# Kernel optimization log

Measured on AMD Instinct MI355X. Metric: run time of the kernel, lower is better.

## Reference

```python
import jax, jax.numpy as jnp
import numpy as np

N_NUM = 8
N_CAT = 4
CARD = 100
D_NUM = 16
D_CAT = 16
D_OUT = N_NUM * D_NUM + N_CAT * D_CAT  # 192
D_HID = 256
TEMP = 1.0


def setup_inputs() -> dict:
    key = jax.random.key(0)
    ks = jax.random.split(key, 12)
    B, N = 512, 131072
    x_num = jax.random.normal(ks[0], (B, N_NUM), dtype=jnp.float32)
    x_cat = jax.random.randint(ks[1], (B, N_CAT), 0, CARD)
    cand_x_num = jax.random.normal(ks[2], (N, N_NUM), dtype=jnp.float32)
    cand_x_cat = jax.random.randint(ks[3], (N, N_CAT), 0, CARD)
    cand_y = jax.random.uniform(ks[4], (N, 10), dtype=jnp.float32)
    s = 0.05
    W_num = jax.random.normal(ks[5], (N_NUM, D_NUM), dtype=jnp.float32) * s
    b_num = jax.random.normal(ks[6], (N_NUM, D_NUM), dtype=jnp.float32) * s
    emb = jax.random.normal(ks[7], (N_CAT, CARD, D_CAT), dtype=jnp.float32) * s
    W1 = jax.random.normal(ks[8], (D_OUT, D_HID), dtype=jnp.float32) * s
    b1 = jnp.zeros((D_HID,), dtype=jnp.float32)
    W2 = jax.random.normal(ks[9], (D_HID, D_OUT), dtype=jnp.float32) * s
    b2 = jnp.zeros((D_OUT,), dtype=jnp.float32)
    return dict(x_num=x_num, x_cat=x_cat, cand_x_num=cand_x_num,
                cand_x_cat=cand_x_cat, cand_y=cand_y, W_num=W_num, b_num=b_num,
                emb=emb, W1=W1, b1=b1, W2=W2, b2=b2)


def _encode(x_num, x_cat, W_num, b_num, emb):
    # per-numerical-feature linear embedding: [B, n_num, d_num]
    num_e = x_num[:, :, None] * W_num[None] + b_num[None]
    # categorical lookup: emb[f, x_cat[:, f]] -> [B, n_cat, d_cat]
    cat_e = emb[jnp.arange(N_CAT)[None, :], x_cat]
    B = x_num.shape[0]
    return jnp.concatenate([num_e.reshape(B, -1), cat_e.reshape(B, -1)], axis=-1)


def _block(z, W1, b1, W2, b2):
    # residual MLP block: d_out -> hidden -> d_out
    return z + jax.nn.relu(z @ W1 + b1) @ W2 + b2


def reference(x_num, x_cat, cand_x_num, cand_x_cat, cand_y,
              W_num, b_num, emb, W1, b1, W2, b2):
    x = _encode(x_num, x_cat, W_num, b_num, emb)            # [B, d]
    c = _encode(cand_x_num, cand_x_cat, W_num, b_num, emb)  # [N, d]
    x = _block(x, W1, b1, W2, b2)
    c = _block(c, W1, b1, W2, b2)
    d2 = (jnp.sum(x * x, axis=-1)[:, None] + jnp.sum(c * c, axis=-1)[None, :]
          - 2.0 * (x @ c.T))
    dist = jnp.sqrt(jnp.maximum(d2, 0.0)) / TEMP            # [B, N]
    probs = jax.nn.softmax(-dist, axis=-1)
    return probs @ cand_y                                    # [B, 10]
```

## Files before the change

### kernel.cpp

```cpp
#include <hip/hip_runtime.h>
#include <hip/hip_bf16.h>

typedef __bf16 bf16;
typedef __attribute__((ext_vector_type(8))) __bf16 bf16x8;
typedef __attribute__((ext_vector_type(4))) __bf16 bf16x4;
typedef __attribute__((ext_vector_type(4))) float f32x4;

#define NQ     512
#define NC     131072
#define DIM    192
#define HID    256
#define NY     10
#define NSLICE 512

#define KL2E   2.0813689810056077f
#define N2KL2E -4.1627379620112154f

#define OFF_W1B 0u
#define OFF_W2B (OFF_W1B + 49152u)
#define OFF_XE8 (OFF_W2B + 49152u)
#define OFF_X2  (OFF_XE8 + 98304u)
#define OFF_CE8 (OFF_X2 + 2048u)
#define OFF_C2  (OFF_CE8 + 25165824u)
#define OFF_ACC (OFF_C2 + 524288u)
#define OFF_YB  (OFF_ACC + 262144u)

static __device__ __forceinline__ unsigned pk4(float a, float b, float c, float d) {
  unsigned w = __builtin_amdgcn_cvt_pk_fp8_f32(a, b, 0, false);
  w = __builtin_amdgcn_cvt_pk_fp8_f32(c, d, w, true);
  return w;
}

__global__ __launch_bounds__(256) void k_prep(const float* __restrict__ W1,
                                              const float* __restrict__ W2,
                                              const float* __restrict__ cy,
                                              unsigned char* __restrict__ W1B8,
                                              unsigned char* __restrict__ W2B8,
                                              bf16* __restrict__ YB,
                                              float* __restrict__ ACC) {
  if (blockIdx.x < 384) {
    int idx = blockIdx.x * 256 + threadIdx.x;
    if (idx < 192 * 256) {
      int k = idx / 256, n = idx % 256;
      int p = (k >> 5) * 4 + ((k >> 3) & 3);
      int pk = __builtin_amdgcn_cvt_pk_fp8_f32(W1[idx], W1[idx], 0, false);
      W1B8[((size_t)(p * 256 + n)) * 8 + (k & 7)] = (unsigned char)(pk & 0xff);
    } else {
      int i2 = idx - 192 * 256;
      int k = i2 / 192, n = i2 % 192;
      int p = (k >> 5) * 4 + ((k >> 3) & 3);
      int pk = __builtin_amdgcn_cvt_pk_fp8_f32(W2[i2], W2[i2], 0, false);
      W2B8[((size_t)(p * 192 + n)) * 8 + (k & 7)] = (unsigned char)(pk & 0xff);
    }
  } else if (blockIdx.x < 1408) {
    int u = (blockIdx.x - 384) * 256 + threadIdx.x;
    int p32 = u >> 6, lane6 = u & 63;
    int qq = lane6 >> 4, l15 = lane6 & 15;
    bf16x8 v;
#pragma unroll
    for (int jj = 0; jj < 8; jj++) {
      int cand = p32 * 32 + qq * 8 + jj;
      float x = (l15 < 10) ? cy[(size_t)cand * NY + l15] : (l15 == 10 ? 1.f : 0.f);
      v[jj] = (bf16)x;
    }
    *(bf16x8*)&YB[(size_t)u * 8] = v;
  } else {
    int idx = (blockIdx.x - 1408) * 256 + threadIdx.x;
    f32x4 z = {0.f, 0.f, 0.f, 0.f};
    *(f32x4*)&ACC[idx * 4] = z;
  }
}

__global__ __launch_bounds__(256, 4) void k_encode(
    const float* __restrict__ xnq, const int* __restrict__ xcq,
    const float* __restrict__ xnc, const int* __restrict__ xcc,
    const float* __restrict__ Wn, const float* __restrict__ bn,
    const float* __restrict__ emb, const float* __restrict__ b1,
    const float* __restrict__ b2, const unsigned char* __restrict__ W1B8,
    const unsigned char* __restrict__ W2B8, unsigned char* __restrict__ ce8,
    unsigned char* __restrict__ xe8, float* __restrict__ x2v,
    float* __restrict__ c2v) {
  __shared__ alignas(16) unsigned char zt8[64][208];
  __shared__ alignas(16) unsigned char hth8[64][264];
  __shared__ float n2l[64];

  const int t = threadIdx.x;
  const bool isq = blockIdx.x < 8;
  const int row0 = (isq ? blockIdx.x : blockIdx.x - 8) * 64;
  const float* __restrict__ xn = isq ? xnq : xnc;
  const int* __restrict__ xc = isq ? xcq : xcc;
  const int lane = t & 63, w = t >> 6;
  const int l15 = lane & 15, q = lane >> 4;

  if (t < 64) n2l[t] = 0.f;

  {
    const int g = row0 + lane;
    float2 xv2 = *(const float2*)&xn[(size_t)g * 8 + 2 * w];
    int cv = xc[g * 4 + w];
#pragma unroll
    for (int f01 = 0; f01 < 2; f01++) {
      int f = 2 * w + f01;
      float xv = f01 ? xv2.y : xv2.x;
      float zz[16];
#pragma unroll
      for (int i = 0; i < 4; i++) {
        f32x4 wv = *(const f32x4*)&Wn[f * 16 + i * 4];
        f32x4 bv = *(const f32x4*)&bn[f * 16 + i * 4];
#pragma unroll
        for (int u = 0; u < 4; u++) zz[i * 4 + u] = xv * wv[u] + bv[u];
      }
      uint4 pk;
      pk.x = pk4(zz[0], zz[1], zz[2], zz[3]);
      pk.y = pk4(zz[4], zz[5], zz[6], zz[7]);
      pk.z = pk4(zz[8], zz[9], zz[10], zz[11]);
      pk.w = pk4(zz[12], zz[13], zz[14], zz[15]);
      *(uint4*)&zt8[lane][f * 16] = pk;
    }
    const float* er = &emb[(size_t)(w * 100 + cv) * 16];
    f32x4 e0 = *(const f32x4*)&er[0];
    f32x4 e1 = *(const f32x4*)&er[4];
    f32x4 e2 = *(const f32x4*)&er[8];
    f32x4 e3 = *(const f32x4*)&er[12];
    uint4 pk;
    pk.x = pk4(e0[0], e0[1], e0[2], e0[3]);
    pk.y = pk4(e1[0], e1[1], e1[2], e1[3]);
    pk.z = pk4(e2[0], e2[1], e2[2], e2[3]);
    pk.w = pk4(e3[0], e3[1], e3[2], e3[3]);
    *(uint4*)&zt8[lane][128 + w * 16] = pk;
  }
  __syncthreads();

  f32x4 z4 = {0.f, 0.f, 0.f, 0.f};

  {
    f32x4 acc1[4][4];
#pragma unroll
    for (int mi = 0; mi < 4; mi++)
#pragma unroll
      for (int ni = 0; ni < 4; ni++) acc1[mi][ni] = z4;
#pragma unroll 2
    for (int kk = 0; kk < 192; kk += 32) {
      long a[4], b[4];
#pragma unroll
      for (int mi = 0; mi < 4; mi++)
        a[mi] = *(const long*)&zt8[mi * 16 + l15][kk + q * 8];
      const unsigned char* wp = &W1B8[(size_t)(((kk >> 5) * 4 + q) * 256 + w * 64 + l15) * 8];
#pragma unroll
      for (int ni = 0; ni < 4; ni++)
        b[ni] = *(const long*)&wp[ni * 128];
#pragma unroll
      for (int mi = 0; mi < 4; mi++)
#pragma unroll
        for (int ni = 0; ni < 4; ni++)
          acc1[mi][ni] = __builtin_amdgcn_mfma_f32_16x16x32_fp8_fp8(b[ni], a[mi], acc1[mi][ni], 0, 0, 0);
    }
#pragma unroll
    for (int ni = 0; ni < 4; ni++) {
      f32x4 bb = *(const f32x4*)&b1[w * 64 + ni * 16 + q * 4];
#pragma unroll
      for (int mi = 0; mi < 4; mi++) {
        float h0 = acc1[mi][ni][0] + bb[0]; h0 = h0 > 0.f ? h0 : 0.f;
        float h1 = acc1[mi][ni][1] + bb[1]; h1 = h1 > 0.f ? h1 : 0.f;
        float h2 = acc1[mi][ni][2] + bb[2]; h2 = h2 > 0.f ? h2 : 0.f;
        float h3 = acc1[mi][ni][3] + bb[3]; h3 = h3 > 0.f ? h3 : 0.f;
        *(unsigned*)&hth8[mi * 16 + l15][w * 64 + ni * 16 + q * 4] = pk4(h0, h1, h2, h3);
      }
    }
  }
  __syncthreads();

  f32x4 acc2[4][3];
#pragma unroll
  for (int mi = 0; mi < 4; mi++)
#pragma unroll
    for (int ni = 0; ni < 3; ni++) acc2[mi][ni] = z4;
#pragma unroll 2
  for (int kk = 0; kk < 256; kk += 32) {
    long a[4], b[3];
#pragma unroll
    for (int mi = 0; mi < 4; mi++)
      a[mi] = *(const long*)&hth8[mi * 16 + l15][kk + q * 8];
    const unsigned char* wp = &W2B8[(size_t)(((kk >> 5) * 4 + q) * 192 + w * 48 + l15) * 8];
#pragma unroll
    for (int ni = 0; ni < 3; ni++)
      b[ni] = *(const long*)&wp[ni * 128];
#pragma unroll
    for (int mi = 0; mi < 4; mi++)
#pragma unroll
      for (int ni = 0; ni < 3; ni++)
        acc2[mi][ni] = __builtin_amdgcn_mfma_f32_16x16x32_fp8_fp8(b[ni], a[mi], acc2[mi][ni], 0, 0, 0);
  }

  {
    float nrm[4];
#pragma unroll
    for (int mi = 0; mi < 4; mi++) nrm[mi] = 0.f;
#pragma unroll
    for (int ni = 0; ni < 3; ni++) {
      const int n0 = w * 48 + ni * 16 + q * 4;
      f32x4 bb = *(const f32x4*)&b2[n0];
#pragma unroll
      for (int mi = 0; mi < 4; mi++) {
        const int rr = mi * 16 + l15;
        unsigned old = *(const unsigned*)&zt8[rr][n0];
        float v0 = __builtin_amdgcn_cvt_f32_fp8((int)old, 0) + acc2[mi][ni][0] + bb[0];
        float v1 = __builtin_amdgcn_cvt_f32_fp8((int)old, 1) + acc2[mi][ni][1] + bb[1];
        float v2 = __builtin_amdgcn_cvt_f32_fp8((int)old, 2) + acc2[mi][ni][2] + bb[2];
        float v3 = __builtin_amdgcn_cvt_f32_fp8((int)old, 3) + acc2[mi][ni][3] + bb[3];
        unsigned pkw = pk4(v0, v1, v2, v3);
        *(unsigned*)&zt8[rr][n0] = pkw;
        float r0 = __builtin_amdgcn_cvt_f32_fp8((int)pkw, 0);
        float r1 = __builtin_amdgcn_cvt_f32_fp8((int)pkw, 1);
        float r2 = __builtin_amdgcn_cvt_f32_fp8((int)pkw, 2);
        float r3 = __builtin_amdgcn_cvt_f32_fp8((int)pkw, 3);
        nrm[mi] += r0 * r0 + r1 * r1 + r2 * r2 + r3 * r3;
      }
    }
#pragma unroll
    for (int mi = 0; mi < 4; mi++) {
      float s = nrm[mi];
      s += __shfl_xor(s, 16);
      s += __shfl_xor(s, 32);
      if (lane < 16) atomicAdd(&n2l[mi * 16 + l15], s);
    }
  }
  __syncthreads();

  if (isq) {
    for (int cc = w; cc < 24; cc += 4) {
      long v = *(const long*)&zt8[lane][cc * 8];
      *(long*)&xe8[((size_t)cc * NQ + row0 + lane) * 8] = v;
    }
    if (t < 64) x2v[row0 + t] = n2l[t] * KL2E;
  } else {
    unsigned int* dst = (unsigned int*)(ce8 + (size_t)row0 * DIM);
#pragma unroll
    for (int i = 0; i < 12; i++) {
      int j = t + 256 * i;
      int r = j / 48, cb = (j - r * 48) * 4;
      dst[j] = *(const unsigned int*)&zt8[r][cb];
    }
    if (t < 64) c2v[row0 + t] = n2l[t] * KL2E;
  }
}

__global__ __launch_bounds__(256, 4) void k_dist(
    const unsigned char* __restrict__ xe8, const float* __restrict__ x2v,
    const unsigned char* __restrict__ ce8, const float* __restrict__ c2v,
    const bf16* __restrict__ YB, float* __restrict__ ACC) {
  __shared__ alignas(16) unsigned char ct8[2][64][208];
  __shared__ alignas(16) bf16 ET[4][16][72];

  const int t = threadIdx.x;
  const int slice = blockIdx.x & (NSLICE - 1);
  const int half = blockIdx.x >> 9;
  const int n0 = slice * 256;
  const int qh = half * 256;
  const int lane = t & 63, w = t >> 6;
  const int l15 = lane & 15, q = lane >> 4;
  const int qbase = qh + w * 64;
  const int sr = t >> 2, squ = t & 3;

  f32x4 z4 = {0.f, 0.f, 0.f, 0.f};
  f32x4 oacc[4];
#pragma unroll
  for (int nq = 0; nq < 4; nq++) oacc[nq] = z4;

  float x2a[4];
#pragma unroll
  for (int nq = 0; nq < 4; nq++) x2a[nq] = x2v[qbase + nq * 16 + l15];

  {
    const uint4* src = (const uint4*)(ce8 + (size_t)(n0 + sr) * DIM + squ * 48);
    uint4* dst = (uint4*)&ct8[0][sr][squ * 48];
#pragma unroll
    for (int i = 0; i < 3; i++) dst[i] = src[i];
  }

#pragma unroll 1
  for (int c = 0; c < 4; ++c) {
    const int cb = c & 1;
    uint4 pf0, pf1, pf2;
    if (c < 3) {
      const uint4* src = (const uint4*)(ce8 + (size_t)(n0 + (c + 1) * 64 + sr) * DIM + squ * 48);
      pf0 = src[0]; pf1 = src[1]; pf2 = src[2];
    }
    __syncthreads();

    f32x4 acc[4][4];
#pragma unroll
    for (int mc = 0; mc < 4; mc++)
#pragma unroll
      for (int nq = 0; nq < 4; nq++) acc[mc][nq] = z4;

#pragma unroll 1
    for (int kk = 0; kk < 192; kk += 32) {
      long a[4], b[4];
#pragma unroll
      for (int mc = 0; mc < 4; mc++)
        a[mc] = *(const long*)&ct8[cb][mc * 16 + l15][kk + q * 8];
      const unsigned char* xp = &xe8[(size_t)(((kk >> 5) * 4 + q) * NQ + qbase + l15) * 8];
#pragma unroll
      for (int nq = 0; nq < 4; nq++)
        b[nq] = *(const long*)&xp[nq * 128];
#pragma unroll
      for (int mc = 0; mc < 4; mc++)
#pragma unroll
        for (int nq = 0; nq < 4; nq++)
          acc[mc][nq] = __builtin_amdgcn_mfma_f32_16x16x32_fp8_fp8(a[mc], b[nq], acc[mc][nq], 0, 0, 0);
    }

    bf16x8 yf[2];
#pragma unroll
    for (int kb = 0; kb < 2; kb++)
      yf[kb] = *(const bf16x8*)&YB[((size_t)((slice * 8) + c * 2 + kb) * 64 + lane) * 8];
    f32x4 c2r[4];
#pragma unroll
    for (int mc = 0; mc < 4; mc++)
      c2r[mc] = *(const f32x4*)&c2v[n0 + c * 64 + mc * 16 + q * 4];

#pragma unroll
    for (int nq = 0; nq < 4; ++nq) {
#pragma unroll
      for (int mc = 0; mc < 4; mc++) {
        bf16x4 ev;
#pragma unroll
        for (int r = 0; r < 4; r++) {
          float d2 = __builtin_fmaf(N2KL2E, acc[mc][nq][r], x2a[nq] + c2r[mc][r]);
          ev[r] = (bf16)__builtin_amdgcn_exp2f(-__builtin_amdgcn_sqrtf(__builtin_fabsf(d2)));
        }
        *(bf16x4*)&ET[w][l15][mc * 16 + q * 4] = ev;
      }
#pragma unroll
      for (int kb = 0; kb < 2; kb++) {
        bf16x8 a = *(const bf16x8*)&ET[w][l15][kb * 32 + q * 8];
        oacc[nq] = __builtin_amdgcn_mfma_f32_16x16x32_bf16(a, yf[kb], oacc[nq], 0, 0, 0);
      }
    }

    if (c < 3) {
      uint4* dst = (uint4*)&ct8[cb ^ 1][sr][squ * 48];
      dst[0] = pf0; dst[1] = pf1; dst[2] = pf2;
    }
  }

  {
    const int i8 = blockIdx.x & 7;
    float* pb = ACC + ((size_t)i8 * NQ + qbase) * 16 + q * 64 + l15;
    if (l15 < 11) {
#pragma unroll
      for (int nq = 0; nq < 4; nq++)
#pragma unroll
        for (int r = 0; r < 4; r++)
          atomicAdd(pb + nq * 256 + r * 16, oacc[nq][r]);
    }
  }
}

__global__ __launch_bounds__(256) void k_norm(const float* __restrict__ ACC,
                                              float* __restrict__ out) {
  int u = blockIdx.x * 256 + threadIdx.x;
  int qy = u >> 4, y = u & 15;
  if (y < 10) {
    float o = 0.f, l = 0.f;
#pragma unroll
    for (int i = 0; i < 8; i++) {
      o += ACC[((size_t)i * NQ + qy) * 16 + y];
      l += ACC[((size_t)i * NQ + qy) * 16 + 10];
    }
    out[qy * NY + y] = o / l;
  }
}

extern "C" void kernel_launch(void* const* d_in, const int* in_sizes, int n_in,
                              void* d_out, int out_size, void* d_ws, size_t ws_size,
                              hipStream_t stream) {
  (void)in_sizes; (void)n_in; (void)out_size; (void)ws_size;
  const float* x_num = (const float*)d_in[0];
  const int*   x_cat = (const int*)d_in[1];
  const float* c_num = (const float*)d_in[2];
  const int*   c_cat = (const int*)d_in[3];
  const float* c_y   = (const float*)d_in[4];
  const float* W_num = (const float*)d_in[5];
  const float* b_num = (const float*)d_in[6];
  const float* emb   = (const float*)d_in[7];
  const float* W1    = (const float*)d_in[8];
  const float* b1    = (const float*)d_in[9];
  const float* W2    = (const float*)d_in[10];
  const float* b2    = (const float*)d_in[11];
  float* out = (float*)d_out;

  char* ws = (char*)d_ws;
  unsigned char* W1B8 = (unsigned char*)(ws + OFF_W1B);
  unsigned char* W2B8 = (unsigned char*)(ws + OFF_W2B);
  unsigned char* xe8  = (unsigned char*)(ws + OFF_XE8);
  float* x2v = (float*)(ws + OFF_X2);
  unsigned char* ce8  = (unsigned char*)(ws + OFF_CE8);
  float* c2v = (float*)(ws + OFF_C2);
  float* ACC = (float*)(ws + OFF_ACC);
  bf16*  YB  = (bf16*)(ws + OFF_YB);

  k_prep<<<dim3(1472), dim3(256), 0, stream>>>(W1, W2, c_y, W1B8, W2B8, YB, ACC);
  k_encode<<<dim3(8 + NC / 64), dim3(256), 0, stream>>>(
      x_num, x_cat, c_num, c_cat, W_num, b_num, emb, b1, b2, W1B8, W2B8,
      ce8, xe8, x2v, c2v);
  k_dist<<<dim3(2 * NSLICE), dim3(256), 0, stream>>>(xe8, x2v, ce8, c2v, YB, ACC);
  k_norm<<<dim3(32), dim3(256), 0, stream>>>(ACC, out);
}
```

Before: 167.0 us.

## Split distance MFMA into halves, remap slices, stage atomics through LDS

The distance GEMM is split into two query halves, so only an 4x2 accumulator tile is live at once. This cuts VGPR pressure, which matters under the 4-waves launch bound. Block-to-slice mapping is permuted so consecutive blocks touch different candidate regions. The final partial sums are transposed through shared memory so each thread issues 11 contiguous atomics instead of scattered ones. The added syncs and LDS traffic are small, but the x operand is now reloaded per half.

```diff
diff --git a/kernel.cpp b/kernel.cpp
--- a/kernel.cpp
+++ b/kernel.cpp
@@ -253,8 +253,10 @@
   __shared__ alignas(16) bf16 ET[4][16][72];
 
   const int t = threadIdx.x;
-  const int slice = blockIdx.x & (NSLICE - 1);
-  const int half = blockIdx.x >> 9;
+  const int raw = blockIdx.x;
+  const int half = raw >> 9;
+  const int r9 = raw & (NSLICE - 1);
+  const int slice = (r9 & 7) * 64 + (r9 >> 3);
   const int n0 = slice * 256;
   const int qh = half * 256;
   const int lane = t & 63, w = t >> 6;
@@ -288,29 +290,6 @@
     }
     __syncthreads();
 
-    f32x4 acc[4][4];
-#pragma unroll
-    for (int mc = 0; mc < 4; mc++)
-#pragma unroll
-      for (int nq = 0; nq < 4; nq++) acc[mc][nq] = z4;
-
-#pragma unroll 1
-    for (int kk = 0; kk < 192; kk += 32) {
-      long a[4], b[4];
-#pragma unroll
-      for (int mc = 0; mc < 4; mc++)
-        a[mc] = *(const long*)&ct8[cb][mc * 16 + l15][kk + q * 8];
-      const unsigned char* xp = &xe8[(size_t)(((kk >> 5) * 4 + q) * NQ + qbase + l15) * 8];
-#pragma unroll
-      for (int nq = 0; nq < 4; nq++)
-        b[nq] = *(const long*)&xp[nq * 128];
-#pragma unroll
-      for (int mc = 0; mc < 4; mc++)
-#pragma unroll
-        for (int nq = 0; nq < 4; nq++)
-          acc[mc][nq] = __builtin_amdgcn_mfma_f32_16x16x32_fp8_fp8(a[mc], b[nq], acc[mc][nq], 0, 0, 0);
-    }
-
     bf16x8 yf[2];
 #pragma unroll
     for (int kb = 0; kb < 2; kb++)
@@ -321,21 +300,48 @@
       c2r[mc] = *(const f32x4*)&c2v[n0 + c * 64 + mc * 16 + q * 4];
 
 #pragma unroll
-    for (int nq = 0; nq < 4; ++nq) {
-#pragma unroll
-      for (int mc = 0; mc < 4; mc++) {
-        bf16x4 ev;
-#pragma unroll
-        for (int r = 0; r < 4; r++) {
-          float d2 = __builtin_fmaf(N2KL2E, acc[mc][nq][r], x2a[nq] + c2r[mc][r]);
-          ev[r] = (bf16)__builtin_amdgcn_exp2f(-__builtin_amdgcn_sqrtf(__builtin_fabsf(d2)));
+    for (int nqh = 0; nqh < 2; nqh++) {
+      f32x4 acc[4][2];
+#pragma unroll
+      for (int mc = 0; mc < 4; mc++)
+#pragma unroll
+        for (int j = 0; j < 2; j++) acc[mc][j] = z4;
+
+#pragma unroll 2
+      for (int kk = 0; kk < 192; kk += 32) {
+        long a[4], b[2];
+#pragma unroll
+        for (int mc = 0; mc < 4; mc++)
+          a[mc] = *(const long*)&ct8[cb][mc * 16 + l15][kk + q * 8];
+        const unsigned char* xp = &xe8[(size_t)(((kk >> 5) * 4 + q) * NQ + qbase + nqh * 32 + l15) * 8];
+#pragma unroll
+        for (int j = 0; j < 2; j++)
+          b[j] = *(const long*)&xp[j * 128];
+#pragma unroll
+        for (int mc = 0; mc < 4; mc++)
+#pragma unroll
+          for (int j = 0; j < 2; j++)
+            acc[mc][j] = __builtin_amdgcn_mfma_f32_16x16x32_fp8_fp8(a[mc], b[j], acc[mc][j], 0, 0, 0);
+      }
+
+#pragma unroll
+      for (int j = 0; j < 2; ++j) {
+        const int nq = nqh * 2 + j;
+#pragma unroll
+        for (int mc = 0; mc < 4; mc++) {
+          bf16x4 ev;
+#pragma unroll
+          for (int r = 0; r < 4; r++) {
+            float d2 = __builtin_fmaf(N2KL2E, acc[mc][j][r], x2a[nq] + c2r[mc][r]);
+            ev[r] = (bf16)__builtin_amdgcn_exp2f(-__builtin_amdgcn_sqrtf(__builtin_fabsf(d2)));
+          }
+          *(bf16x4*)&ET[w][l15][mc * 16 + q * 4] = ev;
         }
-        *(bf16x4*)&ET[w][l15][mc * 16 + q * 4] = ev;
-      }
-#pragma unroll
-      for (int kb = 0; kb < 2; kb++) {
-        bf16x8 a = *(const bf16x8*)&ET[w][l15][kb * 32 + q * 8];
-        oacc[nq] = __builtin_amdgcn_mfma_f32_16x16x32_bf16(a, yf[kb], oacc[nq], 0, 0, 0);
+#pragma unroll
+        for (int kb = 0; kb < 2; kb++) {
+          bf16x8 a = *(const bf16x8*)&ET[w][l15][kb * 32 + q * 8];
+          oacc[nq] = __builtin_amdgcn_mfma_f32_16x16x32_bf16(a, yf[kb], oacc[nq], 0, 0, 0);
+        }
       }
     }
 
@@ -345,16 +351,24 @@
     }
   }
 
+  __syncthreads();
+  float* Pst = (float*)&ct8[0][0][0];
+  if (l15 < 11) {
+#pragma unroll
+    for (int nq = 0; nq < 4; nq++)
+#pragma unroll
+      for (int r = 0; r < 4; r++) {
+        int lq = w * 64 + nq * 16 + q * 4 + r;
+        Pst[lq * 12 + l15] = oacc[nq][r];
+      }
+  }
+  __syncthreads();
   {
-    const int i8 = blockIdx.x & 7;
-    float* pb = ACC + ((size_t)i8 * NQ + qbase) * 16 + q * 64 + l15;
-    if (l15 < 11) {
-#pragma unroll
-      for (int nq = 0; nq < 4; nq++)
-#pragma unroll
-        for (int r = 0; r < 4; r++)
-          atomicAdd(pb + nq * 256 + r * 16, oacc[nq][r]);
-    }
+    const int i8 = raw & 7;
+    float* ab = ACC + ((size_t)i8 * NQ + qh + t) * 16;
+#pragma unroll
+    for (int i = 0; i < 11; i++)
+      atomicAdd(ab + i, Pst[t * 12 + i]);
   }
 }
 
```

New measurement: 373.2 us. 2.24x slower.
